# Optimization experiments

Measured on AMD Instinct MI355X. Metric: run time of the kernel, lower is better.

## Reference

```python
import jax, jax.numpy as jnp
import numpy as np

B, S, H, E, I = 2, 1024, 1024, 8, 512
EPS = 1e-8  # torch F.cosine_similarity eps


def setup_inputs() -> dict:
    key = jax.random.key(0)
    ks = jax.random.split(key, 5)
    return {
        "hidden_states": jax.random.normal(ks[0], (B, S, H), dtype=jnp.float32),
        "expert_embeddings": jax.random.normal(ks[1], (E, H), dtype=jnp.float32),
        # torch init is zeros; -0.03 keeps the zero-selection fallback (which NaNs the
        # original's softmax) from ever triggering while preserving ~half-dense routing
        "gate_threshold": jnp.full((E,), -0.03, dtype=jnp.float32),
        "w_gate": jax.random.normal(ks[2], (E, H, I), dtype=jnp.float32) / np.sqrt(H).astype(np.float32),
        "w_up": jax.random.normal(ks[3], (E, H, I), dtype=jnp.float32) / np.sqrt(H).astype(np.float32),
        "w_down": jax.random.normal(ks[4], (E, I, H), dtype=jnp.float32) / np.sqrt(I).astype(np.float32),
    }


def _forward(hidden_states, expert_embeddings, gate_threshold, w_gate, w_up, w_down):
    b, s, h = hidden_states.shape
    n_experts = expert_embeddings.shape[0]
    x = hidden_states.reshape(-1, h)  # [T, H]

    # cosine-similarity routing scores [T, E]
    xn = x / jnp.maximum(jnp.linalg.norm(x, axis=-1, keepdims=True), EPS)
    en = expert_embeddings / jnp.maximum(jnp.linalg.norm(expert_embeddings, axis=-1, keepdims=True), EPS)
    scores = xn @ en.T

    # SiLUHardThreshold forward: hard 0/1 mask (used only as a boolean downstream,
    # so no gradient flows through it in the module's output path)
    routing_mask = (jax.nn.silu(scores - gate_threshold) > 0).astype(scores.dtype)

    # guarantee at least one expert per token: fall back to top-1 score
    num_sel = routing_mask.sum(axis=-1)  # [T]
    top1 = jnp.argmax(scores, axis=-1)   # [T]
    routing_mask_final = jnp.where((num_sel == 0)[:, None],
                                   jax.nn.one_hot(top1, n_experts, dtype=scores.dtype),
                                   routing_mask)

    # softmax over selected experts (pre-fallback mask, as in the original)
    masked_scores = jnp.where(routing_mask > 0, scores, -jnp.inf)
    routing_weights = jax.nn.softmax(masked_scores.astype(jnp.float32), axis=-1).astype(x.dtype)
    gates = routing_weights * routing_mask_final  # [T, E] combine weights

    # per-expert Qwen3 SwiGLU MLP: down(silu(gate(x)) * up(x)); dense over experts,
    # gated combine is the vectorized equivalent of the gather/MLP/index_add loop
    hmid = jax.nn.silu(jnp.einsum('th,ehi->eti', x, w_gate)) * jnp.einsum('th,ehi->eti', x, w_up)  # [E,T,I]
    out = jnp.einsum('eti,eih,te->th', hmid, w_down, gates)  # [T, H]

    return out.reshape(b, s, h), scores


def reference(hidden_states, expert_embeddings, gate_threshold, w_gate, w_up, w_down):
    # returns (final_hidden_states [B,S,H], router_logits [T,E])
    return _forward(hidden_states, expert_embeddings, gate_threshold, w_gate, w_up, w_down)
```

## Files before the change

kernel.cpp:

```cpp
#include <hip/hip_runtime.h>
#include <hip/hip_bf16.h>
#include <stdint.h>

#define T_TOK 2048
#define H_DIM 1024
#define E_NUM 8
#define I_DIM 512
#define KDOWN (E_NUM * I_DIM)
#define EPSR 1e-8f

typedef short s16x8 __attribute__((ext_vector_type(8)));
typedef float f32x4 __attribute__((ext_vector_type(4)));

static __device__ __forceinline__ uint16_t f2bf(float f) {
    union { float f; uint32_t i; } v; v.f = f;
    uint32_t lsb = (v.i >> 16) & 1u;
    v.i += 0x7fffu + lsb;
    return (uint16_t)(v.i >> 16);
}

static __device__ __forceinline__ void gll16(const void* g, void* l) {
    __builtin_amdgcn_global_load_lds(
        (const __attribute__((address_space(1))) void*)g,
        (__attribute__((address_space(3))) void*)l, 16, 0, 0);
}

__global__ __launch_bounds__(256) void transpose_all_kernel(
    const float* __restrict__ wg, const float* __restrict__ wu,
    const float* __restrict__ wd, uint16_t* __restrict__ wgT,
    uint16_t* __restrict__ wuT, uint16_t* __restrict__ wdT) {
    __shared__ float tile[64][68];
    const int z = blockIdx.z;
    const float* src; uint16_t* dst; int C, out_stride, r0, c0;
    if (z < 16) {
        const int e = z & 7;
        src = (z < 8 ? wg : wu) + (long)e * H_DIM * I_DIM;
        dst = (z < 8 ? wgT : wuT) + (long)e * I_DIM * H_DIM;
        C = I_DIM; out_stride = H_DIM;
        r0 = blockIdx.y * 64; c0 = blockIdx.x * 64;
    } else {
        const int e = z - 16;
        src = wd + (long)e * I_DIM * H_DIM;
        dst = wdT + (long)e * I_DIM;
        C = H_DIM; out_stride = KDOWN;
        r0 = blockIdx.x * 64; c0 = blockIdx.y * 64;
    }
    const int tid = threadIdx.x;
    const int g16 = tid >> 4, l16 = (tid & 15) * 4;
    #pragma unroll
    for (int it = 0; it < 4; ++it) {
        int r = it * 16 + g16;
        *(float4*)&tile[r][l16] = *(const float4*)(src + (long)(r0 + r) * C + c0 + l16);
    }
    __syncthreads();
    #pragma unroll
    for (int it = 0; it < 4; ++it) {
        int oc = it * 16 + g16;
        ushort4 o;
        o.x = f2bf(tile[l16 + 0][oc]);
        o.y = f2bf(tile[l16 + 1][oc]);
        o.z = f2bf(tile[l16 + 2][oc]);
        o.w = f2bf(tile[l16 + 3][oc]);
        *(ushort4*)(dst + (long)(c0 + oc) * out_stride + r0 + l16) = o;
    }
}

__global__ __launch_bounds__(256) void routing_kernel(
    const float* __restrict__ x, const float* __restrict__ emb,
    const float* __restrict__ thr, float* __restrict__ scores_out,
    float* __restrict__ gates, uint16_t* __restrict__ xb) {
    __shared__ float semb[E_NUM * H_DIM];
    __shared__ float senorm[E_NUM];
    const int tid = threadIdx.x;
    const int lane = tid & 63;
    const int wave = tid >> 6;
    for (int i = tid; i < E_NUM * H_DIM; i += 256) semb[i] = emb[i];
    __syncthreads();
    for (int e = wave; e < E_NUM; e += 4) {
        float s = 0.f;
        #pragma unroll
        for (int c = 0; c < 16; ++c) { float v = semb[e * H_DIM + lane + 64 * c]; s += v * v; }
        #pragma unroll
        for (int off = 32; off; off >>= 1) s += __shfl_xor(s, off);
        if (lane == 0) senorm[e] = fmaxf(sqrtf(s), EPSR);
    }
    __syncthreads();
    const int t = blockIdx.x * 4 + wave;
    const float* xt = x + (long)t * H_DIM;
    uint16_t* xbt = xb + (long)t * H_DIM;
    float nrm = 0.f, dot[E_NUM];
    #pragma unroll
    for (int e = 0; e < E_NUM; ++e) dot[e] = 0.f;
    #pragma unroll
    for (int c = 0; c < 16; ++c) {
        float v = xt[lane + 64 * c];
        xbt[lane + 64 * c] = f2bf(v);
        nrm += v * v;
        #pragma unroll
        for (int e = 0; e < E_NUM; ++e) dot[e] += v * semb[e * H_DIM + lane + 64 * c];
    }
    #pragma unroll
    for (int off = 32; off; off >>= 1) {
        nrm += __shfl_xor(nrm, off);
        #pragma unroll
        for (int e = 0; e < E_NUM; ++e) dot[e] += __shfl_xor(dot[e], off);
    }
    float xn = fmaxf(sqrtf(nrm), EPSR);
    float sc[E_NUM], sel[E_NUM];
    float msel = -1e30f, mall = -1e30f;
    int nsel = 0, arg = 0;
    #pragma unroll
    for (int e = 0; e < E_NUM; ++e) {
        sc[e] = dot[e] / (xn * senorm[e]);
        float d = sc[e] - thr[e];
        sel[e] = (d > 0.f) ? 1.f : 0.f;
        if (d > 0.f) { nsel++; msel = fmaxf(msel, sc[e]); }
        if (sc[e] > mall) { mall = sc[e]; arg = e; }
    }
    float w[E_NUM], den = 0.f;
    #pragma unroll
    for (int e = 0; e < E_NUM; ++e) { w[e] = (sel[e] > 0.f) ? __expf(sc[e] - msel) : 0.f; den += w[e]; }
    if (lane == 0) {
        #pragma unroll
        for (int e = 0; e < E_NUM; ++e) {
            scores_out[t * E_NUM + e] = sc[e];
            gates[t * E_NUM + e] = (nsel > 0) ? (w[e] / den) : ((e == arg) ? 1.f : 0.f);
        }
    }
}

__global__ __launch_bounds__(256, 2) void moe_gateup_kernel(
    const uint16_t* __restrict__ xb,
    const uint16_t* __restrict__ wgT,
    const uint16_t* __restrict__ wuT,
    const float* __restrict__ gates,
    uint16_t* __restrict__ hmid) {
    const int e  = blockIdx.z;
    const int t0 = blockIdx.x * 128;
    const int i0 = blockIdx.y * 128;
    __shared__ uint16_t sA[128][64];
    __shared__ uint16_t sG[128][64];
    __shared__ uint16_t sU[128][64];
    __shared__ float sGate[128];
    const int tid  = threadIdx.x;
    const int lane = tid & 63;
    const int wave = tid >> 6;
    const int wm = wave >> 1, wn = wave & 1;
    if (tid < 128) sGate[tid] = gates[(t0 + tid) * E_NUM + e];

    const int srow = wave * 32 + (lane >> 3);
    const int scol = ((lane & 7) ^ (srow & 7)) * 8;
    const uint16_t* ga = xb  + (long)(t0 + srow) * H_DIM + scol;
    const uint16_t* gg = wgT + ((long)e * I_DIM + i0 + srow) * H_DIM + scol;
    const uint16_t* gu = wuT + ((long)e * I_DIM + i0 + srow) * H_DIM + scol;

    f32x4 accg[4][4] = {}, accu[4][4] = {};
    const int q = lane >> 4, r16 = lane & 15;
    const int sw = r16 & 7;

    for (int kb = 0; kb < H_DIM; kb += 64) {
        __syncthreads();
        #pragma unroll
        for (int j = 0; j < 4; ++j) {
            const int lr = wave * 32 + j * 8;
            gll16(ga + (long)j * 8 * H_DIM + kb, &sA[lr][0]);
            gll16(gg + (long)j * 8 * H_DIM + kb, &sG[lr][0]);
            gll16(gu + (long)j * 8 * H_DIM + kb, &sU[lr][0]);
        }
        __syncthreads();
        #pragma unroll
        for (int kk = 0; kk < 2; ++kk) {
            const int pc = ((kk * 4 + q) ^ sw) * 8;
            s16x8 af[4], gf[4], uf[4];
            #pragma unroll
            for (int m = 0; m < 4; ++m)
                af[m] = *(const s16x8*)&sA[wm * 64 + m * 16 + r16][pc];
            #pragma unroll
            for (int n = 0; n < 4; ++n) {
                gf[n] = *(const s16x8*)&sG[wn * 64 + n * 16 + r16][pc];
                uf[n] = *(const s16x8*)&sU[wn * 64 + n * 16 + r16][pc];
            }
            #pragma unroll
            for (int m = 0; m < 4; ++m)
                #pragma unroll
                for (int n = 0; n < 4; ++n) {
                    accg[m][n] = __builtin_amdgcn_mfma_f32_16x16x32_bf16(af[m], gf[n], accg[m][n], 0, 0, 0);
                    accu[m][n] = __builtin_amdgcn_mfma_f32_16x16x32_bf16(af[m], uf[n], accu[m][n], 0, 0, 0);
                }
        }
    }
    #pragma unroll
    for (int m = 0; m < 4; ++m) {
        #pragma unroll
        for (int rr = 0; rr < 4; ++rr) {
            const int trow = wm * 64 + m * 16 + q * 4 + rr;
            const float gate = sGate[trow];
            const long base = (long)(t0 + trow) * KDOWN + e * I_DIM + i0;
            #pragma unroll
            for (int n = 0; n < 4; ++n) {
                float g = accg[m][n][rr], u = accu[m][n][rr];
                float h = gate * (g / (1.f + __expf(-g))) * u;
                hmid[base + wn * 64 + n * 16 + r16] = f2bf(h);
            }
        }
    }
}

__global__ __launch_bounds__(256, 3) void moe_down_kernel(
    const uint16_t* __restrict__ hmid,
    const uint16_t* __restrict__ wdT,
    float* __restrict__ out,
    float* __restrict__ parts) {
    const int t0 = blockIdx.x * 128;
    const int h0 = blockIdx.y * 128;
    const int kz = blockIdx.z;
    const int kst = kz * 1024;
    __shared__ uint16_t sA[128][64];
    __shared__ uint16_t sB[128][64];
    const int tid  = threadIdx.x;
    const int lane = tid & 63;
    const int wave = tid >> 6;
    const int wm = wave >> 1, wn = wave & 1;

    const int srow = wave * 32 + (lane >> 3);
    const int scol = ((lane & 7) ^ (srow & 7)) * 8;
    const uint16_t* ga = hmid + (long)(t0 + srow) * KDOWN + scol;
    const uint16_t* gb = wdT  + (long)(h0 + srow) * KDOWN + scol;

    f32x4 acc[4][4] = {};
    const int q = lane >> 4, r16 = lane & 15;
    const int sw = r16 & 7;

    for (int kb = kst; kb < kst + 1024; kb += 64) {
        __syncthreads();
        #pragma unroll
        for (int j = 0; j < 4; ++j) {
            const int lr = wave * 32 + j * 8;
            gll16(ga + (long)j * 8 * KDOWN + kb, &sA[lr][0]);
            gll16(gb + (long)j * 8 * KDOWN + kb, &sB[lr][0]);
        }
        __syncthreads();
        #pragma unroll
        for (int kk = 0; kk < 2; ++kk) {
            const int pc = ((kk * 4 + q) ^ sw) * 8;
            s16x8 af[4], bf[4];
            #pragma unroll
            for (int m = 0; m < 4; ++m)
                af[m] = *(const s16x8*)&sA[wm * 64 + m * 16 + r16][pc];
            #pragma unroll
            for (int n = 0; n < 4; ++n)
                bf[n] = *(const s16x8*)&sB[wn * 64 + n * 16 + r16][pc];
            #pragma unroll
            for (int m = 0; m < 4; ++m)
                #pragma unroll
                for (int n = 0; n < 4; ++n)
                    acc[m][n] = __builtin_amdgcn_mfma_f32_16x16x32_bf16(af[m], bf[n], acc[m][n], 0, 0, 0);
        }
    }
    float* dst = (kz == 0) ? out : (parts + (long)(kz - 1) * T_TOK * H_DIM);
    #pragma unroll
    for (int m = 0; m < 4; ++m) {
        #pragma unroll
        for (int rr = 0; rr < 4; ++rr) {
            const int t = t0 + wm * 64 + m * 16 + q * 4 + rr;
            #pragma unroll
            for (int n = 0; n < 4; ++n)
                dst[(long)t * H_DIM + h0 + wn * 64 + n * 16 + r16] = acc[m][n][rr];
        }
    }
}

__global__ __launch_bounds__(256) void reduce_kernel(float* __restrict__ out,
                                                     const float* __restrict__ parts) {
    long i = ((long)blockIdx.x * 256 + threadIdx.x) * 4;
    float4 a = *(const float4*)(out + i);
    #pragma unroll
    for (int j = 0; j < 3; ++j) {
        float4 b = *(const float4*)(parts + (long)j * T_TOK * H_DIM + i);
        a.x += b.x; a.y += b.y; a.z += b.z; a.w += b.w;
    }
    *(float4*)(out + i) = a;
}

extern "C" void kernel_launch(void* const* d_in, const int* in_sizes, int n_in,
                              void* d_out, int out_size, void* d_ws, size_t ws_size,
                              hipStream_t stream) {
    const float* x    = (const float*)d_in[0];
    const float* emb  = (const float*)d_in[1];
    const float* thr  = (const float*)d_in[2];
    const float* wg   = (const float*)d_in[3];
    const float* wu   = (const float*)d_in[4];
    const float* wd   = (const float*)d_in[5];
    float* out    = (float*)d_out;
    float* scores = out + (size_t)T_TOK * H_DIM;

    uint8_t* ws = (uint8_t*)d_ws;
    uint16_t* xb   = (uint16_t*)(ws);
    uint16_t* wgT  = (uint16_t*)(ws + (size_t)4  * 1048576);
    uint16_t* wuT  = (uint16_t*)(ws + (size_t)12 * 1048576);
    uint16_t* wdT  = (uint16_t*)(ws + (size_t)20 * 1048576);
    uint16_t* hmid = (uint16_t*)(ws + (size_t)28 * 1048576);
    float*    gates = (float*)  (ws + (size_t)44 * 1048576);
    float*    parts = (float*)  (ws + (size_t)48 * 1048576);

    transpose_all_kernel<<<dim3(8, 16, 24), 256, 0, stream>>>(wg, wu, wd, wgT, wuT, wdT);
    routing_kernel<<<T_TOK / 4, 256, 0, stream>>>(x, emb, thr, scores, gates, xb);
    moe_gateup_kernel<<<dim3(T_TOK / 128, I_DIM / 128, E_NUM), 256, 0, stream>>>(
        xb, wgT, wuT, gates, hmid);
    moe_down_kernel<<<dim3(T_TOK / 128, H_DIM / 128, 4), 256, 0, stream>>>(hmid, wdT, out, parts);
    reduce_kernel<<<(T_TOK * H_DIM) / 1024, 256, 0, stream>>>(out, parts);
}
```

Measured before the change: 178.4 us.

## Merge transpose and routing into one prep kernel, retune gateup occupancy, swap down grid

Weight transpose/bf16 conversion and routing now run as two branches of a single prep kernel over one flat grid. Shared memory is unioned between the two roles. This removes a launch and lets routing blocks overlap with transpose blocks, at the cost of the larger routing shared-memory footprint applying to every block, which may lower occupancy of the transpose blocks. Separately, the gate/up kernel's launch bounds go from 2 to 3 blocks per CU, and the down kernel's grid swaps the token and hidden axes to change block scheduling order and cache reuse.

```diff
diff --git a/kernel.cpp b/kernel.cpp
--- a/kernel.cpp
+++ b/kernel.cpp
@@ -25,67 +25,70 @@
         (__attribute__((address_space(3))) void*)l, 16, 0, 0);
 }
 
-__global__ __launch_bounds__(256) void transpose_all_kernel(
+__global__ __launch_bounds__(256) void prep_kernel(
     const float* __restrict__ wg, const float* __restrict__ wu,
     const float* __restrict__ wd, uint16_t* __restrict__ wgT,
-    uint16_t* __restrict__ wuT, uint16_t* __restrict__ wdT) {
-    __shared__ float tile[64][68];
-    const int z = blockIdx.z;
-    const float* src; uint16_t* dst; int C, out_stride, r0, c0;
-    if (z < 16) {
-        const int e = z & 7;
-        src = (z < 8 ? wg : wu) + (long)e * H_DIM * I_DIM;
-        dst = (z < 8 ? wgT : wuT) + (long)e * I_DIM * H_DIM;
-        C = I_DIM; out_stride = H_DIM;
-        r0 = blockIdx.y * 64; c0 = blockIdx.x * 64;
-    } else {
-        const int e = z - 16;
-        src = wd + (long)e * I_DIM * H_DIM;
-        dst = wdT + (long)e * I_DIM;
-        C = H_DIM; out_stride = KDOWN;
-        r0 = blockIdx.x * 64; c0 = blockIdx.y * 64;
-    }
-    const int tid = threadIdx.x;
-    const int g16 = tid >> 4, l16 = (tid & 15) * 4;
-    #pragma unroll
-    for (int it = 0; it < 4; ++it) {
-        int r = it * 16 + g16;
-        *(float4*)&tile[r][l16] = *(const float4*)(src + (long)(r0 + r) * C + c0 + l16);
-    }
-    __syncthreads();
-    #pragma unroll
-    for (int it = 0; it < 4; ++it) {
-        int oc = it * 16 + g16;
-        ushort4 o;
-        o.x = f2bf(tile[l16 + 0][oc]);
-        o.y = f2bf(tile[l16 + 1][oc]);
-        o.z = f2bf(tile[l16 + 2][oc]);
-        o.w = f2bf(tile[l16 + 3][oc]);
-        *(ushort4*)(dst + (long)(c0 + oc) * out_stride + r0 + l16) = o;
-    }
-}
-
-__global__ __launch_bounds__(256) void routing_kernel(
+    uint16_t* __restrict__ wuT, uint16_t* __restrict__ wdT,
     const float* __restrict__ x, const float* __restrict__ emb,
     const float* __restrict__ thr, float* __restrict__ scores_out,
     float* __restrict__ gates, uint16_t* __restrict__ xb) {
-    __shared__ float semb[E_NUM * H_DIM];
-    __shared__ float senorm[E_NUM];
+    __shared__ union {
+        float tile[64][68];
+        struct { float semb[E_NUM * H_DIM]; float senorm[E_NUM]; } r;
+    } sm;
+    const int bid = blockIdx.x;
     const int tid = threadIdx.x;
+
+    if (bid < 3072) {
+        const int bz = bid >> 7, by = (bid >> 3) & 15, bx = bid & 7;
+        const float* src; uint16_t* dst; int C, out_stride, r0, c0;
+        if (bz < 16) {
+            const int e = bz & 7;
+            src = (bz < 8 ? wg : wu) + (long)e * H_DIM * I_DIM;
+            dst = (bz < 8 ? wgT : wuT) + (long)e * I_DIM * H_DIM;
+            C = I_DIM; out_stride = H_DIM;
+            r0 = by * 64; c0 = bx * 64;
+        } else {
+            const int e = bz - 16;
+            src = wd + (long)e * I_DIM * H_DIM;
+            dst = wdT + (long)e * I_DIM;
+            C = H_DIM; out_stride = KDOWN;
+            r0 = bx * 64; c0 = by * 64;
+        }
+        const int g16 = tid >> 4, l16 = (tid & 15) * 4;
+        #pragma unroll
+        for (int it = 0; it < 4; ++it) {
+            int r = it * 16 + g16;
+            *(float4*)&sm.tile[r][l16] = *(const float4*)(src + (long)(r0 + r) * C + c0 + l16);
+        }
+        __syncthreads();
+        #pragma unroll
+        for (int it = 0; it < 4; ++it) {
+            int oc = it * 16 + g16;
+            ushort4 o;
+            o.x = f2bf(sm.tile[l16 + 0][oc]);
+            o.y = f2bf(sm.tile[l16 + 1][oc]);
+            o.z = f2bf(sm.tile[l16 + 2][oc]);
+            o.w = f2bf(sm.tile[l16 + 3][oc]);
+            *(ushort4*)(dst + (long)(c0 + oc) * out_stride + r0 + l16) = o;
+        }
+        return;
+    }
+    const int rb = bid - 3072;
     const int lane = tid & 63;
     const int wave = tid >> 6;
-    for (int i = tid; i < E_NUM * H_DIM; i += 256) semb[i] = emb[i];
+    for (int i = tid; i < E_NUM * H_DIM; i += 256) sm.r.semb[i] = emb[i];
     __syncthreads();
     for (int e = wave; e < E_NUM; e += 4) {
         float s = 0.f;
         #pragma unroll
-        for (int c = 0; c < 16; ++c) { float v = semb[e * H_DIM + lane + 64 * c]; s += v * v; }
+        for (int c = 0; c < 16; ++c) { float v = sm.r.semb[e * H_DIM + lane + 64 * c]; s += v * v; }
         #pragma unroll
         for (int off = 32; off; off >>= 1) s += __shfl_xor(s, off);
-        if (lane == 0) senorm[e] = fmaxf(sqrtf(s), EPSR);
+        if (lane == 0) sm.r.senorm[e] = fmaxf(sqrtf(s), EPSR);
     }
     __syncthreads();
-    const int t = blockIdx.x * 4 + wave;
+    const int t = rb * 4 + wave;
     const float* xt = x + (long)t * H_DIM;
     uint16_t* xbt = xb + (long)t * H_DIM;
     float nrm = 0.f, dot[E_NUM];
@@ -97,7 +100,7 @@
         xbt[lane + 64 * c] = f2bf(v);
         nrm += v * v;
         #pragma unroll
-        for (int e = 0; e < E_NUM; ++e) dot[e] += v * semb[e * H_DIM + lane + 64 * c];
+        for (int e = 0; e < E_NUM; ++e) dot[e] += v * sm.r.semb[e * H_DIM + lane + 64 * c];
     }
     #pragma unroll
     for (int off = 32; off; off >>= 1) {
@@ -111,7 +114,7 @@
     int nsel = 0, arg = 0;
     #pragma unroll
     for (int e = 0; e < E_NUM; ++e) {
-        sc[e] = dot[e] / (xn * senorm[e]);
+        sc[e] = dot[e] / (xn * sm.r.senorm[e]);
         float d = sc[e] - thr[e];
         sel[e] = (d > 0.f) ? 1.f : 0.f;
         if (d > 0.f) { nsel++; msel = fmaxf(msel, sc[e]); }
@@ -129,7 +132,7 @@
     }
 }
 
-__global__ __launch_bounds__(256, 2) void moe_gateup_kernel(
+__global__ __launch_bounds__(256, 3) void moe_gateup_kernel(
     const uint16_t* __restrict__ xb,
     const uint16_t* __restrict__ wgT,
     const uint16_t* __restrict__ wuT,
@@ -211,8 +214,8 @@
     const uint16_t* __restrict__ wdT,
     float* __restrict__ out,
     float* __restrict__ parts) {
-    const int t0 = blockIdx.x * 128;
-    const int h0 = blockIdx.y * 128;
+    const int h0 = blockIdx.x * 128;
+    const int t0 = blockIdx.y * 128;
     const int kz = blockIdx.z;
     const int kst = kz * 1024;
     __shared__ uint16_t sA[128][64];
@@ -303,10 +306,10 @@
     float*    gates = (float*)  (ws + (size_t)44 * 1048576);
     float*    parts = (float*)  (ws + (size_t)48 * 1048576);
 
-    transpose_all_kernel<<<dim3(8, 16, 24), 256, 0, stream>>>(wg, wu, wd, wgT, wuT, wdT);
-    routing_kernel<<<T_TOK / 4, 256, 0, stream>>>(x, emb, thr, scores, gates, xb);
+    prep_kernel<<<3072 + T_TOK / 4, 256, 0, stream>>>(
+        wg, wu, wd, wgT, wuT, wdT, x, emb, thr, scores, gates, xb);
     moe_gateup_kernel<<<dim3(T_TOK / 128, I_DIM / 128, E_NUM), 256, 0, stream>>>(
         xb, wgT, wuT, gates, hmid);
-    moe_down_kernel<<<dim3(T_TOK / 128, H_DIM / 128, 4), 256, 0, stream>>>(hmid, wdT, out, parts);
+    moe_down_kernel<<<dim3(H_DIM / 128, T_TOK / 128, 4), 256, 0, stream>>>(hmid, wdT, out, parts);
     reduce_kernel<<<(T_TOK * H_DIM) / 1024, 256, 0, stream>>>(out, parts);
 }
```

After: 337.1 us. 89.0% more time.
